# Kernel tuning notes

Hardware: AMD Instinct MI355X
Metric: run time of the kernel (lower is better)

## Reference

```python
import jax, jax.numpy as jnp
import numpy as np

ALPHA = 0.025
BETA = 0.00025
V_TH = 1.0
EXP_TAU = 50.0          # tau_v / dt
T_NOW = 10.0            # current simulation step counter self.t
REFRAC_STEPS = 2        # refractory_period / dt
INV_TAU_V = float(np.exp(-1.0 / 50.0))   # exp(-dt/tau_v)
INV_TAU_I = float(np.exp(-1.0))          # exp(-dt/tau_i)
INV_TAU_V_PAIR = INV_TAU_V               # tau_v_pair defaults to tau_v
INV_TAU_I_PAIR = INV_TAU_I               # tau_i_pair defaults to tau_i

B, N = 32, 4096


def setup_inputs() -> dict:
    key = jax.random.key(0)
    ks = jax.random.split(key, 8)
    return {
        "inp": jax.random.normal(ks[0], (B, N), jnp.float32),
        "W_rec": jax.random.uniform(ks[1], (N, N), jnp.float32),  # nonneg dense adjacency weights
        "mem_pot": jax.random.normal(ks[2], (B, N), jnp.float32),
        "mem_cur": jax.random.normal(ks[3], (B, N), jnp.float32),
        "mem_pot_paired": jax.random.normal(ks[4], (B, N), jnp.float32),
        "mem_cur_paired": jax.random.normal(ks[5], (B, N), jnp.float32),
        "st": jnp.zeros((N,), jnp.float32),
        "refrac_neurons": jax.random.randint(ks[6], (B, N), 0, 3, jnp.int32),
    }


def reference(inp, W_rec, mem_pot, mem_cur, mem_pot_paired, mem_cur_paired, st, refrac_neurons):
    sign_mask = W_rec > 0  # torch: sign(W_rec) > 0 (weights are nonneg)

    # decrement refractory counters
    refrac = jnp.where(refrac_neurons > 0, refrac_neurons - 1, refrac_neurons)

    # threshold (ceil+clamp -> {0,1} spikes)
    S = jnp.clip(jnp.ceil(mem_pot - V_TH), 0.0, 1.0)                     # (B,N)
    S_paired = jnp.clip(jnp.ceil(mem_pot_paired - V_TH - ALPHA), 0.0, 1.0)

    # ---- plasticity weight update ----
    sp_max = S_paired.max(axis=0)            # (N,)
    st_new = jnp.where(S > 0, T_NOW, st)     # broadcasts (N,) -> (B,N), as in torch
    max_st = st_new.max(axis=0)              # (N,)
    # meshgrid(a,b) with ij indexing: |a-b|[i,j] = |max_st[i]-max_st[j]|
    diff = jnp.abs(max_st[:, None] - max_st[None, :])                    # (N,N)
    update_mask = (sp_max[:, None] > 0) & sign_mask                      # (N,N)
    updated = W_rec + BETA - jnp.where(update_mask,
                                       ALPHA * jnp.exp(diff / EXP_TAU),
                                       0.0)
    updated = jnp.clip(updated, 0.0, 1.0)
    W_new = jnp.where(sign_mask, updated, W_rec)

    # ---- integrate ----
    active = refrac == 0
    mem_cur_n = jnp.where(active, inp + S @ W_new + mem_cur, mem_cur)
    mem_cur_p_n = jnp.where(active, S @ W_new.T + mem_cur_paired, mem_cur_paired)
    mem_pot_n = jnp.where(active, mem_cur_n + mem_pot, mem_pot)
    mem_pot_p_n = jnp.where(active, mem_cur_p_n + mem_pot_paired, mem_pot_paired)

    # leak
    mem_pot_n = mem_pot_n * INV_TAU_V
    mem_cur_n = mem_cur_n * INV_TAU_I
    mem_pot_p_n = mem_pot_p_n * INV_TAU_V_PAIR
    mem_cur_p_n = mem_cur_p_n * INV_TAU_I_PAIR

    # reset spiked neurons
    mem_pot_n = jnp.where(S > 0, 0.0, mem_pot_n)
    mem_pot_p_n = jnp.where(S_paired > 0, 0.0, mem_pot_p_n)
    refrac_new = jnp.where(S > 0, REFRAC_STEPS, refrac)

    return S, mem_pot_n, W_new, mem_cur_n, mem_pot_p_n, mem_cur_p_n, refrac_new
```

## Files before the change

### kernel.cpp

```cpp
#include <hip/hip_runtime.h>
#include <cstdint>
#include <cstddef>

constexpr int N = 4096;
constexpr int B = 32;
constexpr int BN = B * N;
constexpr size_t NN = (size_t)N * N;

constexpr int ABLK = 256;
constexpr int BBLK = 512;
constexpr int NPSWT = 8;
constexpr int NPSW = 16;
constexpr int LDTB = 136;

constexpr float ALPHA = 0.025f;
constexpr float BETA = 0.00025f;
constexpr float T_NOW = 10.0f;
constexpr float INV_EXP_TAU = 0.02f;
constexpr float INV_TAU_V = 0.98019867f;
constexpr float INV_TAU_I = 0.36787944f;

typedef __attribute__((ext_vector_type(8))) short short8;
typedef __attribute__((ext_vector_type(4))) float f32x4;

__device__ inline unsigned short f2bf(float f) {
  uint32_t u = __float_as_uint(f);
  u += 0x7FFFu + ((u >> 16) & 1u);
  return (unsigned short)(u >> 16);
}

__device__ inline float wupd(float w, float mrow, float frow, float mcol) {
  float d = fabsf(mrow - mcol);
  float u = w + BETA - frow * __expf(d * INV_EXP_TAU);
  u = fminf(fmaxf(u, 0.0f), 1.0f);
  return (w > 0.0f) ? u : w;
}

__global__ __launch_bounds__(256) void pass_a(
    const float* __restrict__ mem_pot, const float* __restrict__ mem_pot_p,
    const float* __restrict__ st, float* __restrict__ S_out,
    unsigned short* __restrict__ S_bf,
    uint32_t* __restrict__ maskS, uint32_t* __restrict__ maskSP,
    float* __restrict__ max_st, float* __restrict__ rowfac) {
  int j = blockIdx.x * blockDim.x + threadIdx.x;
  if (j >= N) return;
  float stj = st[j];
  uint32_t ms = 0u, msp = 0u;
  float maxv = -3.0e38f;
  #pragma unroll
  for (int b = 0; b < B; ++b) {
    float p = mem_pot[b * N + j];
    float pp = mem_pot_p[b * N + j];
    bool s = (p - 1.0f) > 0.0f;
    bool sp = ((pp - 1.0f) - ALPHA) > 0.0f;
    S_out[b * N + j] = s ? 1.0f : 0.0f;
    S_bf[b * N + j] = s ? 0x3F80u : 0u;
    ms |= (uint32_t)s << b;
    msp |= (uint32_t)sp << b;
    maxv = fmaxf(maxv, s ? T_NOW : stj);
  }
  maskS[j] = ms;
  maskSP[j] = msp;
  max_st[j] = maxv;
  rowfac[j] = msp ? ALPHA : 0.0f;
}

__global__ __launch_bounds__(256, 3) void pass_gemms(
    const float* __restrict__ W, const unsigned short* __restrict__ S_bf,
    const float* __restrict__ max_st, const float* __restrict__ rowfac,
    float* __restrict__ Wout, float* __restrict__ partSW,
    float* __restrict__ partSWT) {
  __shared__ __align__(16) char smem[33792];

  int tid = threadIdx.x;
  int wv = tid >> 6;
  int lane = tid & 63;
  int quad = lane >> 4;
  int nl = lane & 15;
  int row8 = tid >> 5;
  int c4 = tid & 31;

  if (blockIdx.x < ABLK) {
    int it = blockIdx.x & 31;
    int jc = blockIdx.x >> 5;
    int i0 = it * 128;
    float* mstIA = (float*)(smem + 32768);
    float* facIA = mstIA + 128;

    if (tid < 128) {
      mstIA[tid] = max_st[i0 + tid];
      facIA[tid] = rowfac[i0 + tid];
    }

    f32x4 acc[2][2];
    #pragma unroll
    for (int a = 0; a < 2; ++a)
      #pragma unroll
      for (int h = 0; h < 2; ++h) acc[a][h] = (f32x4){0.f, 0.f, 0.f, 0.f};

    __syncthreads();

    #pragma unroll 1
    for (int jsub = 0; jsub < 4; ++jsub) {
      int jb = jc * 512 + jsub * 128;
      float4 pf[16];
      const float* wb = W + (size_t)(i0 + row8) * N + jb + c4 * 4;
      #pragma unroll
      for (int p = 0; p < 16; ++p)
        pf[p] = *(const float4*)(wb + (size_t)(p * 8) * N);
      short8 aA0[4], aA1[4];
      #pragma unroll
      for (int ks = 0; ks < 4; ++ks) {
        int kg = jb + ks * 32 + quad * 8;
        aA0[ks] = *(const short8*)(S_bf + (size_t)nl * N + kg);
        aA1[ks] = *(const short8*)(S_bf + (size_t)(nl + 16) * N + kg);
      }
      float4 mj4 = *(const float4*)(max_st + jb + c4 * 4);

      #pragma unroll
      for (int p = 0; p < 16; ++p) {
        int r = p * 8 + row8;
        float mi = mstIA[r];
        float fi = facIA[r];
        f32x4 u;
        u[0] = wupd(pf[p].x, mi, fi, mj4.x);
        u[1] = wupd(pf[p].y, mi, fi, mj4.y);
        u[2] = wupd(pf[p].z, mi, fi, mj4.z);
        u[3] = wupd(pf[p].w, mi, fi, mj4.w);
        __builtin_nontemporal_store(
            u, (f32x4*)(Wout + (size_t)(i0 + r) * N + jb + c4 * 4));
        uint32_t d0 = (uint32_t)f2bf(u[0]) | ((uint32_t)f2bf(u[1]) << 16);
        uint32_t d1 = (uint32_t)f2bf(u[2]) | ((uint32_t)f2bf(u[3]) << 16);
        uint2 dd; dd.x = d0; dd.y = d1;
        *(uint2*)(smem + r * 256 + ((((c4 >> 1) ^ (r & 7))) << 4) +
                  ((c4 & 1) << 3)) = dd;
      }
      __syncthreads();

      #pragma unroll
      for (int ks = 0; ks < 4; ++ks) {
        #pragma unroll
        for (int nt = 0; nt < 2; ++nt) {
          int rr = wv * 32 + nt * 16 + nl;
          short8 bfr = *(const short8*)(
              smem + rr * 256 + ((((ks * 4 + quad) ^ (rr & 7))) << 4));
          acc[nt][0] =
              __builtin_amdgcn_mfma_f32_16x16x32_bf16(aA0[ks], bfr, acc[nt][0], 0, 0, 0);
          acc[nt][1] =
              __builtin_amdgcn_mfma_f32_16x16x32_bf16(aA1[ks], bfr, acc[nt][1], 0, 0, 0);
        }
      }
      if (jsub < 3) __syncthreads();
    }

    size_t baseA = (size_t)jc * BN;
    #pragma unroll
    for (int nt = 0; nt < 2; ++nt) {
      int ig = i0 + wv * 32 + nt * 16 + nl;
      #pragma unroll
      for (int r = 0; r < 4; ++r) {
        partSWT[baseA + (size_t)(quad * 4 + r) * N + ig] = acc[nt][0][r];
        partSWT[baseA + (size_t)(16 + quad * 4 + r) * N + ig] = acc[nt][1][r];
      }
    }
  } else {
    int idx = blockIdx.x - ABLK;
    int jt = idx & 31;
    int ic = idx >> 5;
    int j0 = jt * 128;
    int ibase = ic * 256;
    unsigned short* tileB = (unsigned short*)smem;
    float* mstIB = (float*)(smem + 17408);
    float* facIB = mstIB + 256;
    float* mstJB = facIB + 256;

    mstIB[tid] = max_st[ibase + tid];
    facIB[tid] = rowfac[ibase + tid];
    if (tid < 128) mstJB[tid] = max_st[j0 + tid];

    float4 pf[8];
    {
      const float* wb = W + (size_t)(ibase + row8) * N + j0 + c4 * 4;
      #pragma unroll
      for (int p = 0; p < 8; ++p)
        pf[p] = *(const float4*)(wb + (size_t)(p * 8) * N);
    }

    f32x4 accB[2][2];
    #pragma unroll
    for (int a = 0; a < 2; ++a)
      #pragma unroll
      for (int h = 0; h < 2; ++h) accB[a][h] = (f32x4){0.f, 0.f, 0.f, 0.f};

    __syncthreads();

    #pragma unroll 1
    for (int isub = 0; isub < 4; ++isub) {
      short8 aB0[2], aB1[2];
      #pragma unroll
      for (int ks = 0; ks < 2; ++ks) {
        int kg = ibase + isub * 64 + ks * 32 + quad * 8;
        aB0[ks] = *(const short8*)(S_bf + (size_t)nl * N + kg);
        aB1[ks] = *(const short8*)(S_bf + (size_t)(nl + 16) * N + kg);
      }
      float4 mjB = *(const float4*)(mstJB + c4 * 4);
      #pragma unroll
      for (int p = 0; p < 8; ++p) {
        int r = p * 8 + row8;
        float mi = mstIB[isub * 64 + r];
        float fi = facIB[isub * 64 + r];
        float ux = wupd(pf[p].x, mi, fi, mjB.x);
        float uy = wupd(pf[p].y, mi, fi, mjB.y);
        float uz = wupd(pf[p].z, mi, fi, mjB.z);
        float uw = wupd(pf[p].w, mi, fi, mjB.w);
        uint32_t d0 = (uint32_t)f2bf(ux) | ((uint32_t)f2bf(uy) << 16);
        uint32_t d1 = (uint32_t)f2bf(uz) | ((uint32_t)f2bf(uw) << 16);
        uint2 dd; dd.x = d0; dd.y = d1;
        *(uint2*)((char*)tileB + r * (LDTB * 2) + c4 * 8) = dd;
      }
      if (isub + 1 < 4) {
        const float* wb =
            W + (size_t)(ibase + (isub + 1) * 64 + row8) * N + j0 + c4 * 4;
        #pragma unroll
        for (int p = 0; p < 8; ++p)
          pf[p] = *(const float4*)(wb + (size_t)(p * 8) * N);
      }
      __syncthreads();

      #pragma unroll
      for (int ks = 0; ks < 2; ++ks) {
        #pragma unroll
        for (int t = 0; t < 2; ++t) {
          int js = wv * 2 + t;
          short8 b;
          #pragma unroll
          for (int e = 0; e < 8; ++e)
            b[e] = (short)tileB[(ks * 32 + quad * 8 + e) * LDTB + js * 16 + nl];
          accB[t][0] =
              __builtin_amdgcn_mfma_f32_16x16x32_bf16(aB0[ks], b, accB[t][0], 0, 0, 0);
          accB[t][1] =
              __builtin_amdgcn_mfma_f32_16x16x32_bf16(aB1[ks], b, accB[t][1], 0, 0, 0);
        }
      }
      if (isub + 1 < 4) __syncthreads();
    }

    size_t baseB = (size_t)ic * BN;
    #pragma unroll
    for (int t = 0; t < 2; ++t) {
      int jg = j0 + (wv * 2 + t) * 16 + nl;
      #pragma unroll
      for (int r = 0; r < 4; ++r) {
        partSW[baseB + (size_t)(quad * 4 + r) * N + jg] = accB[t][0][r];
        partSW[baseB + (size_t)(16 + quad * 4 + r) * N + jg] = accB[t][1][r];
      }
    }
  }
}

__global__ __launch_bounds__(256) void pass_d(
    const float* __restrict__ inp, const float* __restrict__ mem_pot,
    const float* __restrict__ mem_cur, const float* __restrict__ mem_pot_p,
    const float* __restrict__ mem_cur_p, const int* __restrict__ refrac_in,
    const uint32_t* __restrict__ maskS, const uint32_t* __restrict__ maskSP,
    const float* __restrict__ partSW, const float* __restrict__ partSWT,
    float* __restrict__ pot_out, float* __restrict__ cur_out,
    float* __restrict__ potp_out, float* __restrict__ curp_out,
    float* __restrict__ refrac_out) {
  int e = blockIdx.x * 256 + threadIdx.x;
  int b = e >> 12;
  int j = e & (N - 1);

  float SW = 0.0f, SWT = 0.0f;
  #pragma unroll
  for (int c = 0; c < NPSW; ++c) SW += partSW[(size_t)c * BN + e];
  #pragma unroll
  for (int c = 0; c < NPSWT; ++c) SWT += partSWT[(size_t)c * BN + e];

  int r = refrac_in[e];
  int rd = (r > 0) ? (r - 1) : r;
  bool active = (rd == 0);
  bool s = (maskS[j] >> b) & 1u;
  bool sp = (maskSP[j] >> b) & 1u;
  float cur = mem_cur[e], pot = mem_pot[e];
  float curp = mem_cur_p[e], potp = mem_pot_p[e];

  float cur_n = active ? (inp[e] + SW + cur) : cur;
  float curp_n = active ? (SWT + curp) : curp;
  float pot_n = active ? (cur_n + pot) : pot;
  float potp_n = active ? (curp_n + potp) : potp;

  pot_n *= INV_TAU_V;
  cur_n *= INV_TAU_I;
  potp_n *= INV_TAU_V;
  curp_n *= INV_TAU_I;

  if (s) pot_n = 0.0f;
  if (sp) potp_n = 0.0f;
  int rn = s ? 2 : rd;

  pot_out[e] = pot_n;
  cur_out[e] = cur_n;
  potp_out[e] = potp_n;
  curp_out[e] = curp_n;
  refrac_out[e] = (float)rn;
}

extern "C" void kernel_launch(void* const* d_in, const int* in_sizes, int n_in,
                              void* d_out, int out_size, void* d_ws, size_t ws_size,
                              hipStream_t stream) {
  const float* inp = (const float*)d_in[0];
  const float* W = (const float*)d_in[1];
  const float* mem_pot = (const float*)d_in[2];
  const float* mem_cur = (const float*)d_in[3];
  const float* mem_pot_p = (const float*)d_in[4];
  const float* mem_cur_p = (const float*)d_in[5];
  const float* st = (const float*)d_in[6];
  const int* refrac = (const int*)d_in[7];

  float* out = (float*)d_out;
  float* S_out = out;
  float* pot_out = out + BN;
  float* W_out = out + 2 * (size_t)BN;
  float* cur_out = W_out + NN;
  float* potp_out = cur_out + BN;
  float* curp_out = potp_out + BN;
  float* refrac_out = curp_out + BN;

  uint32_t* maskS = (uint32_t*)d_ws;
  uint32_t* maskSP = maskS + N;
  float* max_st = (float*)(maskSP + N);
  float* rowfac = max_st + N;
  unsigned short* S_bf = (unsigned short*)(rowfac + N);
  float* partSW = (float*)(S_bf + BN);
  float* partSWT = partSW + (size_t)NPSW * BN;

  pass_a<<<N / 256, 256, 0, stream>>>(mem_pot, mem_pot_p, st, S_out, S_bf,
                                      maskS, maskSP, max_st, rowfac);
  pass_gemms<<<ABLK + BBLK, 256, 0, stream>>>(W, S_bf, max_st, rowfac,
                                              W_out, partSW, partSWT);
  pass_d<<<BN / 256, 256, 0, stream>>>(inp, mem_pot, mem_cur, mem_pot_p,
                                       mem_cur_p, refrac, maskS, maskSP,
                                       partSW, partSWT, pot_out, cur_out,
                                       potp_out, curp_out, refrac_out);
}
```

Baseline: 155.0 us.

## Split A-path blocks finer, prefetch W tiles across subiterations, use lgkm-only barriers

The W-update/SW^T path now runs twice as many blocks, each covering 256 columns instead of 512, and the partial-sum count grows to match. Each block loads the first half of the next 128x128 W tile into registers before the barrier, so global loads overlap compute and register pressure drops, and occupancy rises to 4 waves per SIMD. __syncthreads is replaced by a barrier that waits only on LDS counters, so outstanding global loads stay in flight across the barrier. The risks are more partial-sum traffic for the reduction and ordering that now relies on the lgkmcnt wait alone.

```diff
diff --git a/kernel.cpp b/kernel.cpp
--- a/kernel.cpp
+++ b/kernel.cpp
@@ -7,9 +7,9 @@
 constexpr int BN = B * N;
 constexpr size_t NN = (size_t)N * N;
 
-constexpr int ABLK = 256;
+constexpr int ABLK = 512;
 constexpr int BBLK = 512;
-constexpr int NPSWT = 8;
+constexpr int NPSWT = 16;
 constexpr int NPSW = 16;
 constexpr int LDTB = 136;
 
@@ -34,6 +34,12 @@
   float u = w + BETA - frow * __expf(d * INV_EXP_TAU);
   u = fminf(fmaxf(u, 0.0f), 1.0f);
   return (w > 0.0f) ? u : w;
+}
+
+__device__ inline void bar_lgkm() {
+  asm volatile("s_waitcnt lgkmcnt(0)" ::: "memory");
+  __builtin_amdgcn_sched_barrier(0);
+  __builtin_amdgcn_s_barrier();
 }
 
 __global__ __launch_bounds__(256) void pass_a(
@@ -65,7 +71,7 @@
   rowfac[j] = msp ? ALPHA : 0.0f;
 }
 
-__global__ __launch_bounds__(256, 3) void pass_gemms(
+__global__ __launch_bounds__(256, 4) void pass_gemms(
     const float* __restrict__ W, const unsigned short* __restrict__ S_bf,
     const float* __restrict__ max_st, const float* __restrict__ rowfac,
     float* __restrict__ Wout, float* __restrict__ partSW,
@@ -92,22 +98,32 @@
       facIA[tid] = rowfac[i0 + tid];
     }
 
+    float4 pfA[8];
+    {
+      const float* wb = W + (size_t)(i0 + row8) * N + jc * 256 + c4 * 4;
+      #pragma unroll
+      for (int p = 0; p < 8; ++p)
+        pfA[p] = *(const float4*)(wb + (size_t)(p * 8) * N);
+    }
+
     f32x4 acc[2][2];
     #pragma unroll
     for (int a = 0; a < 2; ++a)
       #pragma unroll
       for (int h = 0; h < 2; ++h) acc[a][h] = (f32x4){0.f, 0.f, 0.f, 0.f};
 
-    __syncthreads();
+    bar_lgkm();
 
     #pragma unroll 1
-    for (int jsub = 0; jsub < 4; ++jsub) {
-      int jb = jc * 512 + jsub * 128;
-      float4 pf[16];
-      const float* wb = W + (size_t)(i0 + row8) * N + jb + c4 * 4;
-      #pragma unroll
-      for (int p = 0; p < 16; ++p)
-        pf[p] = *(const float4*)(wb + (size_t)(p * 8) * N);
+    for (int jsub = 0; jsub < 2; ++jsub) {
+      int jb = jc * 256 + jsub * 128;
+      float4 pfB2[8];
+      {
+        const float* wb = W + (size_t)(i0 + 64 + row8) * N + jb + c4 * 4;
+        #pragma unroll
+        for (int p = 0; p < 8; ++p)
+          pfB2[p] = *(const float4*)(wb + (size_t)(p * 8) * N);
+      }
       short8 aA0[4], aA1[4];
       #pragma unroll
       for (int ks = 0; ks < 4; ++ks) {
@@ -118,15 +134,15 @@
       float4 mj4 = *(const float4*)(max_st + jb + c4 * 4);
 
       #pragma unroll
-      for (int p = 0; p < 16; ++p) {
+      for (int p = 0; p < 8; ++p) {
         int r = p * 8 + row8;
         float mi = mstIA[r];
         float fi = facIA[r];
         f32x4 u;
-        u[0] = wupd(pf[p].x, mi, fi, mj4.x);
-        u[1] = wupd(pf[p].y, mi, fi, mj4.y);
-        u[2] = wupd(pf[p].z, mi, fi, mj4.z);
-        u[3] = wupd(pf[p].w, mi, fi, mj4.w);
+        u[0] = wupd(pfA[p].x, mi, fi, mj4.x);
+        u[1] = wupd(pfA[p].y, mi, fi, mj4.y);
+        u[2] = wupd(pfA[p].z, mi, fi, mj4.z);
+        u[3] = wupd(pfA[p].w, mi, fi, mj4.w);
         __builtin_nontemporal_store(
             u, (f32x4*)(Wout + (size_t)(i0 + r) * N + jb + c4 * 4));
         uint32_t d0 = (uint32_t)f2bf(u[0]) | ((uint32_t)f2bf(u[1]) << 16);
@@ -135,7 +151,32 @@
         *(uint2*)(smem + r * 256 + ((((c4 >> 1) ^ (r & 7))) << 4) +
                   ((c4 & 1) << 3)) = dd;
       }
-      __syncthreads();
+      #pragma unroll
+      for (int p = 0; p < 8; ++p) {
+        int r = 64 + p * 8 + row8;
+        float mi = mstIA[r];
+        float fi = facIA[r];
+        f32x4 u;
+        u[0] = wupd(pfB2[p].x, mi, fi, mj4.x);
+        u[1] = wupd(pfB2[p].y, mi, fi, mj4.y);
+        u[2] = wupd(pfB2[p].z, mi, fi, mj4.z);
+        u[3] = wupd(pfB2[p].w, mi, fi, mj4.w);
+        __builtin_nontemporal_store(
+            u, (f32x4*)(Wout + (size_t)(i0 + r) * N + jb + c4 * 4));
+        uint32_t d0 = (uint32_t)f2bf(u[0]) | ((uint32_t)f2bf(u[1]) << 16);
+        uint32_t d1 = (uint32_t)f2bf(u[2]) | ((uint32_t)f2bf(u[3]) << 16);
+        uint2 dd; dd.x = d0; dd.y = d1;
+        *(uint2*)(smem + r * 256 + ((((c4 >> 1) ^ (r & 7))) << 4) +
+                  ((c4 & 1) << 3)) = dd;
+      }
+      if (jsub == 0) {
+        const float* wb =
+            W + (size_t)(i0 + row8) * N + jc * 256 + 128 + c4 * 4;
+        #pragma unroll
+        for (int p = 0; p < 8; ++p)
+          pfA[p] = *(const float4*)(wb + (size_t)(p * 8) * N);
+      }
+      bar_lgkm();
 
       #pragma unroll
       for (int ks = 0; ks < 4; ++ks) {
@@ -150,7 +191,7 @@
               __builtin_amdgcn_mfma_f32_16x16x32_bf16(aA1[ks], bfr, acc[nt][1], 0, 0, 0);
         }
       }
-      if (jsub < 3) __syncthreads();
+      if (jsub == 0) bar_lgkm();
     }
 
     size_t baseA = (size_t)jc * BN;
@@ -192,7 +233,7 @@
       #pragma unroll
       for (int h = 0; h < 2; ++h) accB[a][h] = (f32x4){0.f, 0.f, 0.f, 0.f};
 
-    __syncthreads();
+    bar_lgkm();
 
     #pragma unroll 1
     for (int isub = 0; isub < 4; ++isub) {
@@ -225,7 +266,7 @@
         for (int p = 0; p < 8; ++p)
           pf[p] = *(const float4*)(wb + (size_t)(p * 8) * N);
       }
-      __syncthreads();
+      bar_lgkm();
 
       #pragma unroll
       for (int ks = 0; ks < 2; ++ks) {
@@ -242,7 +283,7 @@
               __builtin_amdgcn_mfma_f32_16x16x32_bf16(aB1[ks], b, accB[t][1], 0, 0, 0);
         }
       }
-      if (isub + 1 < 4) __syncthreads();
+      if (isub + 1 < 4) bar_lgkm();
     }
 
     size_t baseB = (size_t)ic * BN;
```

Result: slower. 181.4 us (+17.0%).

## Split weight update into separate pass and run GEMMs on updated weights

Applied to the files above, without the earlier changes.

Moves the plasticity weight update into its own elementwise kernel that writes the new weights, then runs both GEMMs reading the updated weights instead of recomputing the update inline. The transposed-product path now reads rows of the updated weights directly from global memory and converts them to bf16 in registers, dropping its LDS staging and barriers. The other path swaps __syncthreads for a lighter LDS-wait barrier. This removes the duplicated exp/update arithmetic but adds an extra full read of the 64MB weight matrix, relying on cache to absorb it.

```diff
diff --git a/kernel.cpp b/kernel.cpp
--- a/kernel.cpp
+++ b/kernel.cpp
@@ -34,6 +34,12 @@
   float u = w + BETA - frow * __expf(d * INV_EXP_TAU);
   u = fminf(fmaxf(u, 0.0f), 1.0f);
   return (w > 0.0f) ? u : w;
+}
+
+__device__ inline void bar_lgkm() {
+  asm volatile("s_waitcnt lgkmcnt(0)" ::: "memory");
+  __builtin_amdgcn_sched_barrier(0);
+  __builtin_amdgcn_s_barrier();
 }
 
 __global__ __launch_bounds__(256) void pass_a(
@@ -65,32 +71,47 @@
   rowfac[j] = msp ? ALPHA : 0.0f;
 }
 
-__global__ __launch_bounds__(256, 3) void pass_gemms(
-    const float* __restrict__ W, const unsigned short* __restrict__ S_bf,
-    const float* __restrict__ max_st, const float* __restrict__ rowfac,
-    float* __restrict__ Wout, float* __restrict__ partSW,
-    float* __restrict__ partSWT) {
-  __shared__ __align__(16) char smem[33792];
+__global__ __launch_bounds__(256) void pass_b(
+    const float* __restrict__ W, const float* __restrict__ max_st,
+    const float* __restrict__ rowfac, float* __restrict__ Wout) {
+  const float4* __restrict__ W4 = (const float4*)W;
+  float4* __restrict__ Wo4 = (float4*)Wout;
+  const float4* __restrict__ mst4 = (const float4*)max_st;
+  int g0 = blockIdx.x * 256 + threadIdx.x;
+  #pragma unroll
+  for (int it = 0; it < 8; ++it) {
+    int g = g0 + it * (2048 * 256);
+    int i = g >> 10;
+    int jc4 = g & 1023;
+    float4 w = W4[g];
+    float mi = max_st[i];
+    float fi = rowfac[i];
+    float4 mj = mst4[jc4];
+    float4 u;
+    u.x = wupd(w.x, mi, fi, mj.x);
+    u.y = wupd(w.y, mi, fi, mj.y);
+    u.z = wupd(w.z, mi, fi, mj.z);
+    u.w = wupd(w.w, mi, fi, mj.w);
+    Wo4[g] = u;
+  }
+}
+
+__global__ __launch_bounds__(256, 4) void pass_gemm(
+    const float* __restrict__ Wn, const unsigned short* __restrict__ S_bf,
+    float* __restrict__ partSW, float* __restrict__ partSWT) {
+  __shared__ __align__(16) unsigned short tileB[64 * LDTB];
 
   int tid = threadIdx.x;
   int wv = tid >> 6;
   int lane = tid & 63;
   int quad = lane >> 4;
   int nl = lane & 15;
-  int row8 = tid >> 5;
-  int c4 = tid & 31;
 
   if (blockIdx.x < ABLK) {
     int it = blockIdx.x & 31;
     int jc = blockIdx.x >> 5;
     int i0 = it * 128;
-    float* mstIA = (float*)(smem + 32768);
-    float* facIA = mstIA + 128;
-
-    if (tid < 128) {
-      mstIA[tid] = max_st[i0 + tid];
-      facIA[tid] = rowfac[i0 + tid];
-    }
+    int kbase = jc * 512;
 
     f32x4 acc[2][2];
     #pragma unroll
@@ -98,59 +119,37 @@
       #pragma unroll
       for (int h = 0; h < 2; ++h) acc[a][h] = (f32x4){0.f, 0.f, 0.f, 0.f};
 
-    __syncthreads();
-
-    #pragma unroll 1
-    for (int jsub = 0; jsub < 4; ++jsub) {
-      int jb = jc * 512 + jsub * 128;
-      float4 pf[16];
-      const float* wb = W + (size_t)(i0 + row8) * N + jb + c4 * 4;
-      #pragma unroll
-      for (int p = 0; p < 16; ++p)
-        pf[p] = *(const float4*)(wb + (size_t)(p * 8) * N);
-      short8 aA0[4], aA1[4];
-      #pragma unroll
-      for (int ks = 0; ks < 4; ++ks) {
-        int kg = jb + ks * 32 + quad * 8;
-        aA0[ks] = *(const short8*)(S_bf + (size_t)nl * N + kg);
-        aA1[ks] = *(const short8*)(S_bf + (size_t)(nl + 16) * N + kg);
-      }
-      float4 mj4 = *(const float4*)(max_st + jb + c4 * 4);
-
-      #pragma unroll
-      for (int p = 0; p < 16; ++p) {
-        int r = p * 8 + row8;
-        float mi = mstIA[r];
-        float fi = facIA[r];
-        f32x4 u;
-        u[0] = wupd(pf[p].x, mi, fi, mj4.x);
-        u[1] = wupd(pf[p].y, mi, fi, mj4.y);
-        u[2] = wupd(pf[p].z, mi, fi, mj4.z);
-        u[3] = wupd(pf[p].w, mi, fi, mj4.w);
-        __builtin_nontemporal_store(
-            u, (f32x4*)(Wout + (size_t)(i0 + r) * N + jb + c4 * 4));
-        uint32_t d0 = (uint32_t)f2bf(u[0]) | ((uint32_t)f2bf(u[1]) << 16);
-        uint32_t d1 = (uint32_t)f2bf(u[2]) | ((uint32_t)f2bf(u[3]) << 16);
-        uint2 dd; dd.x = d0; dd.y = d1;
-        *(uint2*)(smem + r * 256 + ((((c4 >> 1) ^ (r & 7))) << 4) +
-                  ((c4 & 1) << 3)) = dd;
-      }
-      __syncthreads();
-
-      #pragma unroll
-      for (int ks = 0; ks < 4; ++ks) {
-        #pragma unroll
-        for (int nt = 0; nt < 2; ++nt) {
-          int rr = wv * 32 + nt * 16 + nl;
-          short8 bfr = *(const short8*)(
-              smem + rr * 256 + ((((ks * 4 + quad) ^ (rr & 7))) << 4));
-          acc[nt][0] =
-              __builtin_amdgcn_mfma_f32_16x16x32_bf16(aA0[ks], bfr, acc[nt][0], 0, 0, 0);
-          acc[nt][1] =
-              __builtin_amdgcn_mfma_f32_16x16x32_bf16(aA1[ks], bfr, acc[nt][1], 0, 0, 0);
-        }
-      }
-      if (jsub < 3) __syncthreads();
+    const float* __restrict__ wr0 =
+        Wn + (size_t)(i0 + wv * 32 + nl) * N;
+    const float* __restrict__ wr1 = wr0 + (size_t)16 * N;
+
+    #pragma unroll 2
+    for (int ks = 0; ks < 16; ++ks) {
+      int k = kbase + ks * 32 + quad * 8;
+      short8 a0 = *(const short8*)(S_bf + (size_t)nl * N + k);
+      short8 a1 = *(const short8*)(S_bf + (size_t)(nl + 16) * N + k);
+      {
+        float4 f0 = *(const float4*)(wr0 + k);
+        float4 f1 = *(const float4*)(wr0 + k + 4);
+        short8 b;
+        b[0] = (short)f2bf(f0.x); b[1] = (short)f2bf(f0.y);
+        b[2] = (short)f2bf(f0.z); b[3] = (short)f2bf(f0.w);
+        b[4] = (short)f2bf(f1.x); b[5] = (short)f2bf(f1.y);
+        b[6] = (short)f2bf(f1.z); b[7] = (short)f2bf(f1.w);
+        acc[0][0] = __builtin_amdgcn_mfma_f32_16x16x32_bf16(a0, b, acc[0][0], 0, 0, 0);
+        acc[0][1] = __builtin_amdgcn_mfma_f32_16x16x32_bf16(a1, b, acc[0][1], 0, 0, 0);
+      }
+      {
+        float4 f0 = *(const float4*)(wr1 + k);
+        float4 f1 = *(const float4*)(wr1 + k + 4);
+        short8 b;
+        b[0] = (short)f2bf(f0.x); b[1] = (short)f2bf(f0.y);
+        b[2] = (short)f2bf(f0.z); b[3] = (short)f2bf(f0.w);
+        b[4] = (short)f2bf(f1.x); b[5] = (short)f2bf(f1.y);
+        b[6] = (short)f2bf(f1.z); b[7] = (short)f2bf(f1.w);
+        acc[1][0] = __builtin_amdgcn_mfma_f32_16x16x32_bf16(a0, b, acc[1][0], 0, 0, 0);
+        acc[1][1] = __builtin_amdgcn_mfma_f32_16x16x32_bf16(a1, b, acc[1][1], 0, 0, 0);
+      }
     }
 
     size_t baseA = (size_t)jc * BN;
@@ -169,18 +168,12 @@
     int ic = idx >> 5;
     int j0 = jt * 128;
     int ibase = ic * 256;
-    unsigned short* tileB = (unsigned short*)smem;
-    float* mstIB = (float*)(smem + 17408);
-    float* facIB = mstIB + 256;
-    float* mstJB = facIB + 256;
-
-    mstIB[tid] = max_st[ibase + tid];
-    facIB[tid] = rowfac[ibase + tid];
-    if (tid < 128) mstJB[tid] = max_st[j0 + tid];
+    int row8 = tid >> 5;
+    int c4 = tid & 31;
 
     float4 pf[8];
     {
-      const float* wb = W + (size_t)(ibase + row8) * N + j0 + c4 * 4;
+      const float* wb = Wn + (size_t)(ibase + row8) * N + j0 + c4 * 4;
       #pragma unroll
       for (int p = 0; p < 8; ++p)
         pf[p] = *(const float4*)(wb + (size_t)(p * 8) * N);
@@ -191,8 +184,6 @@
     for (int a = 0; a < 2; ++a)
       #pragma unroll
       for (int h = 0; h < 2; ++h) accB[a][h] = (f32x4){0.f, 0.f, 0.f, 0.f};
-
-    __syncthreads();
 
     #pragma unroll 1
     for (int isub = 0; isub < 4; ++isub) {
@@ -203,29 +194,22 @@
         aB0[ks] = *(const short8*)(S_bf + (size_t)nl * N + kg);
         aB1[ks] = *(const short8*)(S_bf + (size_t)(nl + 16) * N + kg);
       }
-      float4 mjB = *(const float4*)(mstJB + c4 * 4);
       #pragma unroll
       for (int p = 0; p < 8; ++p) {
         int r = p * 8 + row8;
-        float mi = mstIB[isub * 64 + r];
-        float fi = facIB[isub * 64 + r];
-        float ux = wupd(pf[p].x, mi, fi, mjB.x);
-        float uy = wupd(pf[p].y, mi, fi, mjB.y);
-        float uz = wupd(pf[p].z, mi, fi, mjB.z);
-        float uw = wupd(pf[p].w, mi, fi, mjB.w);
-        uint32_t d0 = (uint32_t)f2bf(ux) | ((uint32_t)f2bf(uy) << 16);
-        uint32_t d1 = (uint32_t)f2bf(uz) | ((uint32_t)f2bf(uw) << 16);
+        uint32_t d0 = (uint32_t)f2bf(pf[p].x) | ((uint32_t)f2bf(pf[p].y) << 16);
+        uint32_t d1 = (uint32_t)f2bf(pf[p].z) | ((uint32_t)f2bf(pf[p].w) << 16);
         uint2 dd; dd.x = d0; dd.y = d1;
         *(uint2*)((char*)tileB + r * (LDTB * 2) + c4 * 8) = dd;
       }
       if (isub + 1 < 4) {
         const float* wb =
-            W + (size_t)(ibase + (isub + 1) * 64 + row8) * N + j0 + c4 * 4;
+            Wn + (size_t)(ibase + (isub + 1) * 64 + row8) * N + j0 + c4 * 4;
         #pragma unroll
         for (int p = 0; p < 8; ++p)
           pf[p] = *(const float4*)(wb + (size_t)(p * 8) * N);
       }
-      __syncthreads();
+      bar_lgkm();
 
       #pragma unroll
       for (int ks = 0; ks < 2; ++ks) {
@@ -242,7 +226,7 @@
               __builtin_amdgcn_mfma_f32_16x16x32_bf16(aB1[ks], b, accB[t][1], 0, 0, 0);
         }
       }
-      if (isub + 1 < 4) __syncthreads();
+      if (isub + 1 < 4) bar_lgkm();
     }
 
     size_t baseB = (size_t)ic * BN;
@@ -337,8 +321,8 @@
 
   pass_a<<<N / 256, 256, 0, stream>>>(mem_pot, mem_pot_p, st, S_out, S_bf,
                                       maskS, maskSP, max_st, rowfac);
-  pass_gemms<<<ABLK + BBLK, 256, 0, stream>>>(W, S_bf, max_st, rowfac,
-                                              W_out, partSW, partSWT);
+  pass_b<<<2048, 256, 0, stream>>>(W, max_st, rowfac, W_out);
+  pass_gemm<<<ABLK + BBLK, 256, 0, stream>>>(W_out, S_bf, partSW, partSWT);
   pass_d<<<BN / 256, 256, 0, stream>>>(inp, mem_pot, mem_cur, mem_pot_p,
                                        mem_cur_p, refrac, maskS, maskSP,
                                        partSW, partSWT, pot_out, cur_out,
```

Result: slower. 167.4 us (+8.0%).

## Double-buffer W tile prefetch in GEMM A path, shrink LDS, use lighter barriers

Applied to the files above, without the earlier changes.

The A-path loop now works on 64-column sub-tiles instead of 128 and is fully unrolled, with ping-pong register buffers so the global load of the next W sub-tile is issued before the current one is updated and fed to MFMA. Halving the tile cuts LDS use to about 20KB, and launch bounds move to 4 blocks per CU to raise occupancy. __syncthreads is replaced by a custom barrier that waits only on lgkmcnt, so outstanding global loads are not drained at each barrier. The cost is more register pressure from two prefetch buffers under a tighter occupancy target, and more barrier rounds per block.

```diff
diff --git a/kernel.cpp b/kernel.cpp
--- a/kernel.cpp
+++ b/kernel.cpp
@@ -34,6 +34,13 @@
   float u = w + BETA - frow * __expf(d * INV_EXP_TAU);
   u = fminf(fmaxf(u, 0.0f), 1.0f);
   return (w > 0.0f) ? u : w;
+}
+
+__device__ inline void bar_lgkm() {
+  asm volatile("s_waitcnt lgkmcnt(0)" ::: "memory");
+  __builtin_amdgcn_sched_barrier(0);
+  __builtin_amdgcn_s_barrier();
+  __builtin_amdgcn_sched_barrier(0);
 }
 
 __global__ __launch_bounds__(256) void pass_a(
@@ -65,26 +72,26 @@
   rowfac[j] = msp ? ALPHA : 0.0f;
 }
 
-__global__ __launch_bounds__(256, 3) void pass_gemms(
+__global__ __launch_bounds__(256, 4) void pass_gemms(
     const float* __restrict__ W, const unsigned short* __restrict__ S_bf,
     const float* __restrict__ max_st, const float* __restrict__ rowfac,
     float* __restrict__ Wout, float* __restrict__ partSW,
     float* __restrict__ partSWT) {
-  __shared__ __align__(16) char smem[33792];
+  __shared__ __align__(16) char smem[19968];
 
   int tid = threadIdx.x;
   int wv = tid >> 6;
   int lane = tid & 63;
   int quad = lane >> 4;
   int nl = lane & 15;
-  int row8 = tid >> 5;
-  int c4 = tid & 31;
 
   if (blockIdx.x < ABLK) {
     int it = blockIdx.x & 31;
     int jc = blockIdx.x >> 5;
     int i0 = it * 128;
-    float* mstIA = (float*)(smem + 32768);
+    int c4b = tid & 15;
+    int rowX = tid >> 4;
+    float* mstIA = (float*)(smem + 16384);
     float* facIA = mstIA + 128;
 
     if (tid < 128) {
@@ -98,60 +105,76 @@
       #pragma unroll
       for (int h = 0; h < 2; ++h) acc[a][h] = (f32x4){0.f, 0.f, 0.f, 0.f};
 
-    __syncthreads();
-
-    #pragma unroll 1
-    for (int jsub = 0; jsub < 4; ++jsub) {
-      int jb = jc * 512 + jsub * 128;
-      float4 pf[16];
-      const float* wb = W + (size_t)(i0 + row8) * N + jb + c4 * 4;
-      #pragma unroll
-      for (int p = 0; p < 16; ++p)
-        pf[p] = *(const float4*)(wb + (size_t)(p * 8) * N);
-      short8 aA0[4], aA1[4];
-      #pragma unroll
-      for (int ks = 0; ks < 4; ++ks) {
+    float4 pfA[8], pfB[8];
+    int jb0 = jc * 512;
+    {
+      const float* wb = W + (size_t)(i0 + rowX) * N + jb0 + c4b * 4;
+      #pragma unroll
+      for (int p = 0; p < 8; ++p)
+        pfA[p] = *(const float4*)(wb + (size_t)(p * 16) * N);
+    }
+
+    bar_lgkm();
+
+    auto iterA = [&](int jb, int jbn, float4 (&pfc)[8], float4 (&pfn)[8],
+                     bool pre, bool last) {
+      if (pre) {
+        const float* wb = W + (size_t)(i0 + rowX) * N + jbn + c4b * 4;
+        #pragma unroll
+        for (int p = 0; p < 8; ++p)
+          pfn[p] = *(const float4*)(wb + (size_t)(p * 16) * N);
+      }
+      short8 aA0[2], aA1[2];
+      #pragma unroll
+      for (int ks = 0; ks < 2; ++ks) {
         int kg = jb + ks * 32 + quad * 8;
         aA0[ks] = *(const short8*)(S_bf + (size_t)nl * N + kg);
         aA1[ks] = *(const short8*)(S_bf + (size_t)(nl + 16) * N + kg);
       }
-      float4 mj4 = *(const float4*)(max_st + jb + c4 * 4);
-
-      #pragma unroll
-      for (int p = 0; p < 16; ++p) {
-        int r = p * 8 + row8;
+      float4 mj4 = *(const float4*)(max_st + jb + c4b * 4);
+      #pragma unroll
+      for (int p = 0; p < 8; ++p) {
+        int r = p * 16 + rowX;
         float mi = mstIA[r];
         float fi = facIA[r];
         f32x4 u;
-        u[0] = wupd(pf[p].x, mi, fi, mj4.x);
-        u[1] = wupd(pf[p].y, mi, fi, mj4.y);
-        u[2] = wupd(pf[p].z, mi, fi, mj4.z);
-        u[3] = wupd(pf[p].w, mi, fi, mj4.w);
+        u[0] = wupd(pfc[p].x, mi, fi, mj4.x);
+        u[1] = wupd(pfc[p].y, mi, fi, mj4.y);
+        u[2] = wupd(pfc[p].z, mi, fi, mj4.z);
+        u[3] = wupd(pfc[p].w, mi, fi, mj4.w);
         __builtin_nontemporal_store(
-            u, (f32x4*)(Wout + (size_t)(i0 + r) * N + jb + c4 * 4));
+            u, (f32x4*)(Wout + (size_t)(i0 + r) * N + jb + c4b * 4));
         uint32_t d0 = (uint32_t)f2bf(u[0]) | ((uint32_t)f2bf(u[1]) << 16);
         uint32_t d1 = (uint32_t)f2bf(u[2]) | ((uint32_t)f2bf(u[3]) << 16);
         uint2 dd; dd.x = d0; dd.y = d1;
-        *(uint2*)(smem + r * 256 + ((((c4 >> 1) ^ (r & 7))) << 4) +
-                  ((c4 & 1) << 3)) = dd;
-      }
-      __syncthreads();
-
-      #pragma unroll
-      for (int ks = 0; ks < 4; ++ks) {
+        *(uint2*)(smem + r * 128 + ((((c4b >> 1) ^ (r & 7))) << 4) +
+                  ((c4b & 1) << 3)) = dd;
+      }
+      bar_lgkm();
+      #pragma unroll
+      for (int ks = 0; ks < 2; ++ks) {
         #pragma unroll
         for (int nt = 0; nt < 2; ++nt) {
           int rr = wv * 32 + nt * 16 + nl;
           short8 bfr = *(const short8*)(
-              smem + rr * 256 + ((((ks * 4 + quad) ^ (rr & 7))) << 4));
+              smem + rr * 128 + ((((ks * 4 + quad) ^ (rr & 7))) << 4));
           acc[nt][0] =
               __builtin_amdgcn_mfma_f32_16x16x32_bf16(aA0[ks], bfr, acc[nt][0], 0, 0, 0);
           acc[nt][1] =
               __builtin_amdgcn_mfma_f32_16x16x32_bf16(aA1[ks], bfr, acc[nt][1], 0, 0, 0);
         }
       }
-      if (jsub < 3) __syncthreads();
-    }
+      if (!last) bar_lgkm();
+    };
+
+    iterA(jb0 +   0, jb0 +  64, pfA, pfB, true , false);
+    iterA(jb0 +  64, jb0 + 128, pfB, pfA, true , false);
+    iterA(jb0 + 128, jb0 + 192, pfA, pfB, true , false);
+    iterA(jb0 + 192, jb0 + 256, pfB, pfA, true , false);
+    iterA(jb0 + 256, jb0 + 320, pfA, pfB, true , false);
+    iterA(jb0 + 320, jb0 + 384, pfB, pfA, true , false);
+    iterA(jb0 + 384, jb0 + 448, pfA, pfB, true , false);
+    iterA(jb0 + 448, 0,         pfB, pfA, false, true );
 
     size_t baseA = (size_t)jc * BN;
     #pragma unroll
@@ -169,6 +192,8 @@
     int ic = idx >> 5;
     int j0 = jt * 128;
     int ibase = ic * 256;
+    int row8 = tid >> 5;
+    int c4 = tid & 31;
     unsigned short* tileB = (unsigned short*)smem;
     float* mstIB = (float*)(smem + 17408);
     float* facIB = mstIB + 256;
@@ -192,7 +217,7 @@
       #pragma unroll
       for (int h = 0; h < 2; ++h) accB[a][h] = (f32x4){0.f, 0.f, 0.f, 0.f};
 
-    __syncthreads();
+    bar_lgkm();
 
     #pragma unroll 1
     for (int isub = 0; isub < 4; ++isub) {
@@ -225,7 +250,7 @@
         for (int p = 0; p < 8; ++p)
           pf[p] = *(const float4*)(wb + (size_t)(p * 8) * N);
       }
-      __syncthreads();
+      bar_lgkm();
 
       #pragma unroll
       for (int ks = 0; ks < 2; ++ks) {
@@ -242,7 +267,7 @@
               __builtin_amdgcn_mfma_f32_16x16x32_bf16(aB1[ks], b, accB[t][1], 0, 0, 0);
         }
       }
-      if (isub + 1 < 4) __syncthreads();
+      if (isub + 1 < 4) bar_lgkm();
     }
 
     size_t baseB = (size_t)ic * BN;
```

Result: slower. 167.4 us (+8.0%).
